# Kernel tuning notes

Measured on AMD Instinct MI355X. Metric: run time of the kernel, lower is better.

Reference implementation:

```python
import jax, jax.numpy as jnp
import numpy as np


def setup_inputs() -> dict:
    key = jax.random.key(0)
    k1, k2, k3 = jax.random.split(key, 3)
    d = 256
    x = jax.random.normal(k1, (8, 2048, d), dtype=jnp.float32)
    # torch nn.Linear(d, d, bias=False) weights, shape [out, in]
    Wq = jax.random.normal(k2, (d, d), dtype=jnp.float32) * (d ** -0.5)
    Wk = jax.random.normal(k3, (d, d), dtype=jnp.float32) * (d ** -0.5)
    return {"x": x, "Wq": Wq, "Wk": Wk}


def reference(x, Wq, Wk):
    # q = x @ Wq^T, k = x @ Wk^T (torch Linear convention), v = x (raw context)
    d = x.shape[-1]
    scale = d ** -0.5
    q = jnp.einsum('bnd,ed->bne', x, Wq)
    k = jnp.einsum('bnd,ed->bne', x, Wk)
    sim = jnp.einsum('bid,bjd->bij', q, k) * scale  # [b, n, n]
    attn = jax.nn.softmax(sim, axis=-1)
    out = jnp.einsum('bij,bjd->bid', attn, x)
    return out
```

## Files before the change

kernel.cpp:

```cpp
#include <hip/hip_runtime.h>
#include <hip/hip_bf16.h>

#define BB 8
#define NN 2048
#define DD 256

typedef _Float16 half8 __attribute__((ext_vector_type(8)));
typedef _Float16 half4 __attribute__((ext_vector_type(4)));
typedef float f32x4 __attribute__((ext_vector_type(4)));
typedef unsigned int uint4v __attribute__((ext_vector_type(4)));

#define GLDS(gsrc, ldst) __builtin_amdgcn_global_load_lds( \
    (const __attribute__((address_space(1))) void*)(gsrc), \
    (__attribute__((address_space(3))) void*)(ldst), 16, 0, 0)

__device__ __forceinline__ half8 cvt8(const float* __restrict__ p) {
    f32x4 a = *(const f32x4*)p;
    f32x4 b = *(const f32x4*)(p + 4);
    half8 h;
    h[0] = (_Float16)a[0]; h[1] = (_Float16)a[1];
    h[2] = (_Float16)a[2]; h[3] = (_Float16)a[3];
    h[4] = (_Float16)b[0]; h[5] = (_Float16)b[1];
    h[6] = (_Float16)b[2]; h[7] = (_Float16)b[3];
    return h;
}

__global__ void __launch_bounds__(256)
qk_proj(const float* __restrict__ x, const float* __restrict__ Wq,
        const float* __restrict__ Wk, _Float16* __restrict__ qh,
        _Float16* __restrict__ kh, _Float16* __restrict__ xT) {
    __shared__ __align__(16) _Float16 Wql[16][264];
    __shared__ __align__(16) _Float16 Wkl[16][264];
    const int tid = threadIdx.x;
    const int wave = tid >> 6, lane = tid & 63;
    const int g = lane >> 4, l16 = lane & 15;
    const int rowblk = blockIdx.x >> 1, thalf = blockIdx.x & 1;
    const size_t r0 = ((size_t)rowblk * 4 + wave) * 16;

    half8 xa[8];
#pragma unroll
    for (int c = 0; c < 8; ++c)
        xa[c] = cvt8(x + (r0 + l16) * DD + c * 32 + g * 8);

    {
        const int gt = (int)(r0 + l16);
        const int bb = gt >> 11, nn = gt & 2047;
        _Float16* xtb = xT + (size_t)bb * DD * NN + nn;
        if (thalf == 0) {
#pragma unroll
            for (int c = 0; c < 4; ++c)
#pragma unroll
                for (int j = 0; j < 8; ++j)
                    xtb[(size_t)(c * 32 + g * 8 + j) * NN] = xa[c][j];
        } else {
#pragma unroll
            for (int c = 4; c < 8; ++c)
#pragma unroll
                for (int j = 0; j < 8; ++j)
                    xtb[(size_t)(c * 32 + g * 8 + j) * NN] = xa[c][j];
        }
    }

    for (int i = 0; i < 8; ++i) {
        const int t = thalf * 8 + i;
        __syncthreads();
        {
            const int sel = tid >> 7;
            const int tt  = tid & 127;
            const int row = tt >> 3;
            const int col = (tt & 7) * 32;
            const float* src = (sel ? Wk : Wq) + (size_t)(t * 16 + row) * DD + col;
            _Float16* dst = sel ? &Wkl[row][col] : &Wql[row][col];
#pragma unroll
            for (int j = 0; j < 4; ++j)
                *(half8*)(dst + j * 8) = cvt8(src + j * 8);
        }
        __syncthreads();
        f32x4 aq = {0.f, 0.f, 0.f, 0.f}, ak = {0.f, 0.f, 0.f, 0.f};
#pragma unroll
        for (int c = 0; c < 8; ++c) {
            half8 bq = *(const half8*)&Wql[l16][c * 32 + g * 8];
            half8 bk = *(const half8*)&Wkl[l16][c * 32 + g * 8];
            aq = __builtin_amdgcn_mfma_f32_16x16x32_f16(xa[c], bq, aq, 0, 0, 0);
            ak = __builtin_amdgcn_mfma_f32_16x16x32_f16(xa[c], bk, ak, 0, 0, 0);
        }
#pragma unroll
        for (int r = 0; r < 4; ++r) {
            size_t row = r0 + g * 4 + r;
            qh[row * DD + t * 16 + l16] = (_Float16)(aq[r] * 0.0625f);
            kh[row * DD + t * 16 + l16] = (_Float16)ak[r];
        }
    }
}

__global__ void __launch_bounds__(256, 2)
attn(const _Float16* __restrict__ qh, const _Float16* __restrict__ kh,
     const _Float16* __restrict__ xT, float* __restrict__ out,
     _Float16* __restrict__ Op, float* __restrict__ ml, int lgS) {
    __shared__ __align__(16) _Float16 Kl[2][32 * 256];
    __shared__ __align__(16) _Float16 Vl[2][256 * 32];
    const int tid = threadIdx.x;
    const int wave = tid >> 6, lane = tid & 63;
    const int g = lane >> 4, l16 = lane & 15;
    const int S = 1 << lgS;
    const int b = blockIdx.x & 7;
    const int tt = blockIdx.x >> 3;
    const int s = tt & (S - 1);
    const int qb = tt >> lgS;
    const int wq0 = qb * 128 + wave * 32;
    const int kvlen = NN >> lgS;
    const int kv_begin = s * kvlen;
    const int kv_end = kv_begin + kvlen;

    const _Float16* qp = qh + ((size_t)b * NN + wq0) * DD;
    const _Float16* kb = kh + (size_t)b * NN * DD;
    const _Float16* vb = xT + (size_t)b * DD * NN;

    int krow[4], koff[4], vrow[4];
#pragma unroll
    for (int j = 0; j < 4; ++j) {
        int rp = 4 * j + wave;
        int T = 2 * rp + (lane >> 5);
        krow[j] = 8 * ((T >> 2) & 3) + 4 * (T >> 4) + (T & 3);
        koff[j] = ((lane & 31) * 8) ^ ((T & 7) << 3);
        vrow[j] = 16 * rp + (lane >> 2);
    }
    const int voff = (lane & 3) * 8;

    half8 qf[2][8];
#pragma unroll
    for (int t = 0; t < 2; ++t)
#pragma unroll
        for (int c = 0; c < 8; ++c)
            qf[t][c] = *(const half8*)(qp + (size_t)(t * 16 + l16) * DD + c * 32 + g * 8);

    f32x4 O[2][16];
    f32x4 zero = {0.f, 0.f, 0.f, 0.f};
#pragma unroll
    for (int t = 0; t < 2; ++t)
#pragma unroll
        for (int dt = 0; dt < 16; ++dt) O[t][dt] = zero;
    float m[2] = {-1e30f, -1e30f};
    float l[2] = {0.f, 0.f};

#pragma unroll
    for (int j = 0; j < 4; ++j) {
        int rp = 4 * j + wave;
        GLDS(kb + (size_t)(kv_begin + krow[j]) * DD + koff[j], &Kl[0][rp * 512]);
        GLDS(vb + (size_t)vrow[j] * NN + kv_begin + voff, &Vl[0][rp * 512]);
    }
    __syncthreads();

    int cur = 0;
    for (int kv0 = kv_begin; kv0 < kv_end; kv0 += 32) {
        const int nxt = kv0 + 32;
        if (nxt < kv_end) {
#pragma unroll
            for (int j = 0; j < 4; ++j) {
                int rp = 4 * j + wave;
                GLDS(kb + (size_t)(nxt + krow[j]) * DD + koff[j], &Kl[cur ^ 1][rp * 512]);
                GLDS(vb + (size_t)vrow[j] * NN + nxt + voff, &Vl[cur ^ 1][rp * 512]);
            }
        }
        const _Float16* Klb = Kl[cur];
        const _Float16* Vlb = Vl[cur];

        f32x4 s00 = zero, s01 = zero, s10 = zero, s11 = zero;
        const int swz = (l16 & 7) << 3;
        __builtin_amdgcn_s_setprio(1);
#pragma unroll
        for (int c = 0; c < 8; ++c) {
            int u = (c * 32 + g * 8) ^ swz;
            half8 k0 = *(const half8*)&Klb[l16 * 256 + u];
            half8 k1 = *(const half8*)&Klb[(16 + l16) * 256 + u];
            s00 = __builtin_amdgcn_mfma_f32_16x16x32_f16(k0, qf[0][c], s00, 0, 0, 0);
            s01 = __builtin_amdgcn_mfma_f32_16x16x32_f16(k1, qf[0][c], s01, 0, 0, 0);
            s10 = __builtin_amdgcn_mfma_f32_16x16x32_f16(k0, qf[1][c], s10, 0, 0, 0);
            s11 = __builtin_amdgcn_mfma_f32_16x16x32_f16(k1, qf[1][c], s11, 0, 0, 0);
        }
        __builtin_amdgcn_s_setprio(0);

        float tm[2];
#pragma unroll
        for (int t = 0; t < 2; ++t) {
            const f32x4& a = t ? s10 : s00;
            const f32x4& c = t ? s11 : s01;
            float v = fmaxf(fmaxf(fmaxf(a[0], a[1]), fmaxf(a[2], a[3])),
                            fmaxf(fmaxf(c[0], c[1]), fmaxf(c[2], c[3])));
            v = fmaxf(v, __shfl_xor(v, 16));
            v = fmaxf(v, __shfl_xor(v, 32));
            tm[t] = v;
        }
        bool need = (tm[0] > m[0] + 8.f) || (tm[1] > m[1] + 8.f);
        if (__ballot(need)) {
#pragma unroll
            for (int t = 0; t < 2; ++t) {
                float nm = fmaxf(m[t], tm[t]);
                float al = __expf(m[t] - nm);
                m[t] = nm;
                l[t] *= al;
                float alr[4];
#pragma unroll
                for (int r = 0; r < 4; ++r) alr[r] = __shfl(al, g * 4 + r);
#pragma unroll
                for (int dt = 0; dt < 16; ++dt)
#pragma unroll
                    for (int r = 0; r < 4; ++r) O[t][dt][r] *= alr[r];
            }
        }

        half8 pa[2];
#pragma unroll
        for (int t = 0; t < 2; ++t) {
            f32x4 e0, e1;
            const f32x4& a = t ? s10 : s00;
            const f32x4& c = t ? s11 : s01;
#pragma unroll
            for (int r = 0; r < 4; ++r) {
                e0[r] = __expf(a[r] - m[t]);
                e1[r] = __expf(c[r] - m[t]);
            }
            float rs = (e0[0] + e0[1]) + (e0[2] + e0[3]) +
                       (e1[0] + e1[1]) + (e1[2] + e1[3]);
            rs += __shfl_xor(rs, 16);
            rs += __shfl_xor(rs, 32);
            l[t] += rs;

            uint4v w;
            w[0] = __builtin_bit_cast(unsigned, __builtin_amdgcn_cvt_pkrtz(e0[0], e0[1]));
            w[1] = __builtin_bit_cast(unsigned, __builtin_amdgcn_cvt_pkrtz(e0[2], e0[3]));
            w[2] = __builtin_bit_cast(unsigned, __builtin_amdgcn_cvt_pkrtz(e1[0], e1[1]));
            w[3] = __builtin_bit_cast(unsigned, __builtin_amdgcn_cvt_pkrtz(e1[2], e1[3]));
            pa[t] = __builtin_bit_cast(half8, w);
        }

        __builtin_amdgcn_s_setprio(1);
#pragma unroll
        for (int dt = 0; dt < 16; ++dt) {
            half8 vf = *(const half8*)&Vlb[(dt * 16 + l16) * 32 + g * 8];
            O[0][dt] = __builtin_amdgcn_mfma_f32_16x16x32_f16(pa[0], vf, O[0][dt], 0, 0, 0);
            O[1][dt] = __builtin_amdgcn_mfma_f32_16x16x32_f16(pa[1], vf, O[1][dt], 0, 0, 0);
        }
        __builtin_amdgcn_s_setprio(0);

        __syncthreads();
        cur ^= 1;
    }

    if (lgS == 0) {
#pragma unroll
        for (int t = 0; t < 2; ++t) {
            float rl = 1.0f / l[t];
            float rlr[4];
#pragma unroll
            for (int r = 0; r < 4; ++r) rlr[r] = __shfl(rl, g * 4 + r);
            float* ob = out + ((size_t)b * NN + wq0 + t * 16) * DD;
#pragma unroll
            for (int dt = 0; dt < 16; ++dt)
#pragma unroll
                for (int r = 0; r < 4; ++r)
                    ob[(size_t)(g * 4 + r) * DD + dt * 16 + l16] = O[t][dt][r] * rlr[r];
        }
    } else {
#pragma unroll
        for (int t = 0; t < 2; ++t) {
            float rl = 1.0f / l[t];
            float rlr[4];
#pragma unroll
            for (int r = 0; r < 4; ++r) rlr[r] = __shfl(rl, g * 4 + r);
            _Float16* ow = Op + (((size_t)s * BB + b) * NN + wq0 + t * 16) * DD;
#pragma unroll
            for (int dt = 0; dt < 16; ++dt)
#pragma unroll
                for (int r = 0; r < 4; ++r)
                    ow[(dt * 4 + r) * 64 + lane] = (_Float16)(O[t][dt][r] * rlr[r]);
        }
        if (lane < 16) {
            float* mlp = ml + (((size_t)s * BB + b) * NN + wq0) * 2;
#pragma unroll
            for (int t = 0; t < 2; ++t) {
                mlp[(t * 16 + lane) * 2]     = m[t];
                mlp[(t * 16 + lane) * 2 + 1] = l[t];
            }
        }
    }
}

__global__ void __launch_bounds__(256)
combine(const _Float16* __restrict__ Op, const float* __restrict__ ml,
        float* __restrict__ out, int S) {
    const int b = blockIdx.x & 7;
    const int k = blockIdx.x >> 3;
    const int row = b * NN + k * 4 + (threadIdx.x >> 6);
    const int c0  = (threadIdx.x & 63) * 4;
    const int widx = ((c0 >> 4) * 4 + (row & 3)) * 64 + ((row >> 2) & 3) * 16 + (c0 & 15);
    const size_t rbase = (size_t)(row & ~15) * DD + widx;

    float M = -1e30f;
    for (int s = 0; s < S; ++s)
        M = fmaxf(M, ml[((size_t)s * BB * NN + row) * 2]);
    float wsum = 0.f;
    f32x4 acc = {0.f, 0.f, 0.f, 0.f};
    for (int s = 0; s < S; ++s) {
        const float* mlp = ml + ((size_t)s * BB * NN + row) * 2;
        float w = __expf(mlp[0] - M) * mlp[1];
        wsum += w;
        half4 o = *(const half4*)(Op + (size_t)s * BB * NN * DD + rbase);
        acc[0] += w * (float)o[0]; acc[1] += w * (float)o[1];
        acc[2] += w * (float)o[2]; acc[3] += w * (float)o[3];
    }
    float inv = 1.0f / wsum;
    f32x4 res = {acc[0] * inv, acc[1] * inv, acc[2] * inv, acc[3] * inv};
    *(f32x4*)(out + (size_t)row * DD + c0) = res;
}

extern "C" void kernel_launch(void* const* d_in, const int* in_sizes, int n_in,
                              void* d_out, int out_size, void* d_ws, size_t ws_size,
                              hipStream_t stream) {
    const float* x  = (const float*)d_in[0];
    const float* Wq = (const float*)d_in[1];
    const float* Wk = (const float*)d_in[2];
    float* out = (float*)d_out;

    const size_t NTOK = (size_t)BB * NN;
    const size_t HBUF = NTOK * DD * sizeof(_Float16);
    _Float16* qh = (_Float16*)d_ws;
    _Float16* kh = qh + NTOK * DD;
    _Float16* xT = kh + NTOK * DD;
    const size_t base = 3 * HBUF;
    const size_t OSZ  = NTOK * DD * sizeof(_Float16);
    const size_t MLSZ = NTOK * 2 * sizeof(float);

    int lgS = 0;
    if (ws_size >= base + 4 * (OSZ + MLSZ)) lgS = 2;
    else if (ws_size >= base + 2 * (OSZ + MLSZ)) lgS = 1;
    const int S = 1 << lgS;

    _Float16* Op = (_Float16*)((char*)d_ws + base);
    float* ml = (float*)((char*)d_ws + base + (size_t)S * OSZ);

    qk_proj<<<dim3(BB * NN / 64 * 2), dim3(256), 0, stream>>>(x, Wq, Wk, qh, kh, xT);
    attn<<<dim3(BB * (NN / 128) * S), dim3(256), 0, stream>>>(qh, kh, xT, out, Op, ml, lgS);
    if (S > 1)
        combine<<<dim3(BB * NN / 4), dim3(256), 0, stream>>>(Op, ml, out, S);
}
```

Baseline: 101.7 us.

## Single-buffer V tile, raise KV split to 8, quarter projection work per block

The attention kernel now keeps V in a single LDS buffer. Its load for the next tile is issued after the PV MMAs finish, and an extra barrier is added before PV, which cuts LDS use so more blocks can fit on a CU. The host allows a split-KV factor of 8 when the workspace is large enough, which launches more attention blocks and shortens each KV range at the cost of a heavier combine pass. The projection kernel is split four ways instead of two, so more blocks each compute fewer output tiles, at the cost of reloading x per block.

```diff
diff --git a/kernel.cpp b/kernel.cpp
--- a/kernel.cpp
+++ b/kernel.cpp
@@ -34,7 +34,7 @@
     const int tid = threadIdx.x;
     const int wave = tid >> 6, lane = tid & 63;
     const int g = lane >> 4, l16 = lane & 15;
-    const int rowblk = blockIdx.x >> 1, thalf = blockIdx.x & 1;
+    const int rowblk = blockIdx.x & 255, tq = blockIdx.x >> 8;
     const size_t r0 = ((size_t)rowblk * 4 + wave) * 16;
 
     half8 xa[8];
@@ -46,23 +46,18 @@
         const int gt = (int)(r0 + l16);
         const int bb = gt >> 11, nn = gt & 2047;
         _Float16* xtb = xT + (size_t)bb * DD * NN + nn;
-        if (thalf == 0) {
-#pragma unroll
-            for (int c = 0; c < 4; ++c)
+#pragma unroll
+        for (int c = 0; c < 8; ++c) {
+            if ((c >> 1) == tq) {
 #pragma unroll
                 for (int j = 0; j < 8; ++j)
                     xtb[(size_t)(c * 32 + g * 8 + j) * NN] = xa[c][j];
-        } else {
-#pragma unroll
-            for (int c = 4; c < 8; ++c)
-#pragma unroll
-                for (int j = 0; j < 8; ++j)
-                    xtb[(size_t)(c * 32 + g * 8 + j) * NN] = xa[c][j];
-        }
-    }
-
-    for (int i = 0; i < 8; ++i) {
-        const int t = thalf * 8 + i;
+            }
+        }
+    }
+
+    for (int i = 0; i < 4; ++i) {
+        const int t = tq * 4 + i;
         __syncthreads();
         {
             const int sel = tid >> 7;
@@ -98,7 +93,7 @@
      const _Float16* __restrict__ xT, float* __restrict__ out,
      _Float16* __restrict__ Op, float* __restrict__ ml, int lgS) {
     __shared__ __align__(16) _Float16 Kl[2][32 * 256];
-    __shared__ __align__(16) _Float16 Vl[2][256 * 32];
+    __shared__ __align__(16) _Float16 Vl[256 * 32];
     const int tid = threadIdx.x;
     const int wave = tid >> 6, lane = tid & 63;
     const int g = lane >> 4, l16 = lane & 15;
@@ -147,7 +142,7 @@
     for (int j = 0; j < 4; ++j) {
         int rp = 4 * j + wave;
         GLDS(kb + (size_t)(kv_begin + krow[j]) * DD + koff[j], &Kl[0][rp * 512]);
-        GLDS(vb + (size_t)vrow[j] * NN + kv_begin + voff, &Vl[0][rp * 512]);
+        GLDS(vb + (size_t)vrow[j] * NN + kv_begin + voff, &Vl[rp * 512]);
     }
     __syncthreads();
 
@@ -159,11 +154,9 @@
             for (int j = 0; j < 4; ++j) {
                 int rp = 4 * j + wave;
                 GLDS(kb + (size_t)(nxt + krow[j]) * DD + koff[j], &Kl[cur ^ 1][rp * 512]);
-                GLDS(vb + (size_t)vrow[j] * NN + nxt + voff, &Vl[cur ^ 1][rp * 512]);
             }
         }
         const _Float16* Klb = Kl[cur];
-        const _Float16* Vlb = Vl[cur];
 
         f32x4 s00 = zero, s01 = zero, s10 = zero, s11 = zero;
         const int swz = (l16 & 7) << 3;
@@ -234,16 +227,26 @@
             pa[t] = __builtin_bit_cast(half8, w);
         }
 
+        __syncthreads();
+
         __builtin_amdgcn_s_setprio(1);
 #pragma unroll
         for (int dt = 0; dt < 16; ++dt) {
-            half8 vf = *(const half8*)&Vlb[(dt * 16 + l16) * 32 + g * 8];
+            half8 vf = *(const half8*)&Vl[(dt * 16 + l16) * 32 + g * 8];
             O[0][dt] = __builtin_amdgcn_mfma_f32_16x16x32_f16(pa[0], vf, O[0][dt], 0, 0, 0);
             O[1][dt] = __builtin_amdgcn_mfma_f32_16x16x32_f16(pa[1], vf, O[1][dt], 0, 0, 0);
         }
         __builtin_amdgcn_s_setprio(0);
 
         __syncthreads();
+
+        if (nxt < kv_end) {
+#pragma unroll
+            for (int j = 0; j < 4; ++j) {
+                int rp = 4 * j + wave;
+                GLDS(vb + (size_t)vrow[j] * NN + nxt + voff, &Vl[rp * 512]);
+            }
+        }
         cur ^= 1;
     }
 
@@ -332,14 +335,15 @@
     const size_t MLSZ = NTOK * 2 * sizeof(float);
 
     int lgS = 0;
-    if (ws_size >= base + 4 * (OSZ + MLSZ)) lgS = 2;
+    if (ws_size >= base + 8 * (OSZ + MLSZ)) lgS = 3;
+    else if (ws_size >= base + 4 * (OSZ + MLSZ)) lgS = 2;
     else if (ws_size >= base + 2 * (OSZ + MLSZ)) lgS = 1;
     const int S = 1 << lgS;
 
     _Float16* Op = (_Float16*)((char*)d_ws + base);
     float* ml = (float*)((char*)d_ws + base + (size_t)S * OSZ);
 
-    qk_proj<<<dim3(BB * NN / 64 * 2), dim3(256), 0, stream>>>(x, Wq, Wk, qh, kh, xT);
+    qk_proj<<<dim3(BB * NN / 64 * 4), dim3(256), 0, stream>>>(x, Wq, Wk, qh, kh, xT);
     attn<<<dim3(BB * (NN / 128) * S), dim3(256), 0, stream>>>(qh, kh, xT, out, Op, ml, lgS);
     if (S > 1)
         combine<<<dim3(BB * NN / 4), dim3(256), 0, stream>>>(Op, ml, out, S);
```

New measurement: 122.7 us. 20.6% more time.

## Software-pipeline attention loop: overlap QK^T of next tile with PV of previous

Applied to the files above, without the earlier changes.

Restructures the attention main loop into a skewed pipeline. Each iteration computes QK^T for tile tau, the PV product for tile tau-1, and then the softmax for tau, using ping-pong P registers and a third V buffer in LDS so the prefetch does not overwrite V that is still being read. The goal is to let the matrix-core work and the softmax math overlap and hide latency. It also drops the min-2-blocks launch bound and the setprio hints, which may raise register use and lower occupancy.

```diff
diff --git a/kernel.cpp b/kernel.cpp
--- a/kernel.cpp
+++ b/kernel.cpp
@@ -93,12 +93,12 @@
     }
 }
 
-__global__ void __launch_bounds__(256, 2)
+__global__ void __launch_bounds__(256)
 attn(const _Float16* __restrict__ qh, const _Float16* __restrict__ kh,
      const _Float16* __restrict__ xT, float* __restrict__ out,
      _Float16* __restrict__ Op, float* __restrict__ ml, int lgS) {
     __shared__ __align__(16) _Float16 Kl[2][32 * 256];
-    __shared__ __align__(16) _Float16 Vl[2][256 * 32];
+    __shared__ __align__(16) _Float16 Vl[3][256 * 32];
     const int tid = threadIdx.x;
     const int wave = tid >> 6, lane = tid & 63;
     const int g = lane >> 4, l16 = lane & 15;
@@ -110,7 +110,7 @@
     const int wq0 = qb * 128 + wave * 32;
     const int kvlen = NN >> lgS;
     const int kv_begin = s * kvlen;
-    const int kv_end = kv_begin + kvlen;
+    const int nt = kvlen >> 5;
 
     const _Float16* qp = qh + ((size_t)b * NN + wq0) * DD;
     const _Float16* kb = kh + (size_t)b * NN * DD;
@@ -142,32 +142,13 @@
         for (int dt = 0; dt < 16; ++dt) O[t][dt] = zero;
     float m[2] = {-1e30f, -1e30f};
     float l[2] = {0.f, 0.f};
-
-#pragma unroll
-    for (int j = 0; j < 4; ++j) {
-        int rp = 4 * j + wave;
-        GLDS(kb + (size_t)(kv_begin + krow[j]) * DD + koff[j], &Kl[0][rp * 512]);
-        GLDS(vb + (size_t)vrow[j] * NN + kv_begin + voff, &Vl[0][rp * 512]);
-    }
-    __syncthreads();
-
-    int cur = 0;
-    for (int kv0 = kv_begin; kv0 < kv_end; kv0 += 32) {
-        const int nxt = kv0 + 32;
-        if (nxt < kv_end) {
-#pragma unroll
-            for (int j = 0; j < 4; ++j) {
-                int rp = 4 * j + wave;
-                GLDS(kb + (size_t)(nxt + krow[j]) * DD + koff[j], &Kl[cur ^ 1][rp * 512]);
-                GLDS(vb + (size_t)vrow[j] * NN + nxt + voff, &Vl[cur ^ 1][rp * 512]);
-            }
-        }
-        const _Float16* Klb = Kl[cur];
-        const _Float16* Vlb = Vl[cur];
-
-        f32x4 s00 = zero, s01 = zero, s10 = zero, s11 = zero;
+    half8 paA[2], paB[2];
+
+    f32x4 s00, s01, s10, s11;
+    auto qkt = [&](int tau) {
+        const _Float16* Klb = Kl[tau & 1];
+        s00 = zero; s01 = zero; s10 = zero; s11 = zero;
         const int swz = (l16 & 7) << 3;
-        __builtin_amdgcn_s_setprio(1);
 #pragma unroll
         for (int c = 0; c < 8; ++c) {
             int u = (c * 32 + g * 8) ^ swz;
@@ -178,8 +159,19 @@
             s10 = __builtin_amdgcn_mfma_f32_16x16x32_f16(k0, qf[1][c], s10, 0, 0, 0);
             s11 = __builtin_amdgcn_mfma_f32_16x16x32_f16(k1, qf[1][c], s11, 0, 0, 0);
         }
-        __builtin_amdgcn_s_setprio(0);
-
+    };
+
+    auto pv = [&](int tau, half8 (&paIn)[2]) {
+        const _Float16* Vlb = Vl[tau % 3];
+#pragma unroll
+        for (int dt = 0; dt < 16; ++dt) {
+            half8 vf = *(const half8*)&Vlb[(dt * 16 + l16) * 32 + g * 8];
+            O[0][dt] = __builtin_amdgcn_mfma_f32_16x16x32_f16(paIn[0], vf, O[0][dt], 0, 0, 0);
+            O[1][dt] = __builtin_amdgcn_mfma_f32_16x16x32_f16(paIn[1], vf, O[1][dt], 0, 0, 0);
+        }
+    };
+
+    auto smax = [&](half8 (&paOut)[2]) {
         float tm[2];
 #pragma unroll
         for (int t = 0; t < 2; ++t) {
@@ -208,8 +200,6 @@
                     for (int r = 0; r < 4; ++r) O[t][dt][r] *= alr[r];
             }
         }
-
-        half8 pa[2];
 #pragma unroll
         for (int t = 0; t < 2; ++t) {
             f32x4 e0, e1;
@@ -231,21 +221,44 @@
             w[1] = __builtin_bit_cast(unsigned, __builtin_amdgcn_cvt_pkrtz(e0[2], e0[3]));
             w[2] = __builtin_bit_cast(unsigned, __builtin_amdgcn_cvt_pkrtz(e1[0], e1[1]));
             w[3] = __builtin_bit_cast(unsigned, __builtin_amdgcn_cvt_pkrtz(e1[2], e1[3]));
-            pa[t] = __builtin_bit_cast(half8, w);
-        }
-
-        __builtin_amdgcn_s_setprio(1);
-#pragma unroll
-        for (int dt = 0; dt < 16; ++dt) {
-            half8 vf = *(const half8*)&Vlb[(dt * 16 + l16) * 32 + g * 8];
-            O[0][dt] = __builtin_amdgcn_mfma_f32_16x16x32_f16(pa[0], vf, O[0][dt], 0, 0, 0);
-            O[1][dt] = __builtin_amdgcn_mfma_f32_16x16x32_f16(pa[1], vf, O[1][dt], 0, 0, 0);
-        }
-        __builtin_amdgcn_s_setprio(0);
-
+            paOut[t] = __builtin_bit_cast(half8, w);
+        }
+    };
+
+    auto issue = [&](int tau) {
+        _Float16* kdst = Kl[tau & 1];
+        _Float16* vdst = Vl[tau % 3];
+        const int kvn = kv_begin + (tau << 5);
+#pragma unroll
+        for (int j = 0; j < 4; ++j) {
+            int rp = 4 * j + wave;
+            GLDS(kb + (size_t)(kvn + krow[j]) * DD + koff[j], kdst + rp * 512);
+            GLDS(vb + (size_t)vrow[j] * NN + kvn + voff,      vdst + rp * 512);
+        }
+    };
+
+    auto body = [&](int tau, half8 (&paIn)[2], half8 (&paOut)[2]) {
         __syncthreads();
-        cur ^= 1;
-    }
+        if (tau + 1 < nt) issue(tau + 1);
+        qkt(tau);
+        pv(tau - 1, paIn);
+        smax(paOut);
+    };
+
+    issue(0);
+    __syncthreads();
+    issue(1);
+    qkt(0);
+    smax(paA);
+
+    int tau = 1;
+    for (; tau + 1 < nt - 1; tau += 2) {
+        body(tau, paA, paB);
+        body(tau + 1, paB, paA);
+    }
+    body(nt - 1, paA, paB);
+
+    pv(nt - 1, paB);
 
     if (lgS == 0) {
 #pragma unroll
```

After: 102.7 us. About the same (+1.0%).
